# Kernel tuning notes

Hardware: AMD Instinct MI355X
Metric: run time of the kernel (lower is better)

The kernel has to match this reference:

```python
import jax, jax.numpy as jnp
import numpy as np

B, T, D_MODEL, N_HEAD = 1, 2048, 768, 12
D_HEAD = D_MODEL // N_HEAD
D_HID = 4 * D_MODEL
EPS = 1e-6
ROPE_BASE = 10000.0


def _rms(x):
    # F.rms_norm with no learned weight (pre-norm, modded-nanogpt style)
    return x * jax.lax.rsqrt(jnp.mean(x * x, axis=-1, keepdims=True) + EPS)


def _rope(x, cos, sin):
    # x: (B, T, H, Dh); cos/sin: (1, T, 1, Dh//2)
    d = x.shape[-1] // 2
    x1, x2 = x[..., :d], x[..., d:]
    return jnp.concatenate([x1 * cos + x2 * sin, -x1 * sin + x2 * cos], axis=-1)


def setup_inputs() -> dict:
    key = jax.random.key(0)
    ks = jax.random.split(key, 11)
    w = lambda k, shape: (jax.random.normal(k, shape, jnp.float32) * 0.02)
    return {
        "x": jax.random.normal(ks[0], (B, T, D_MODEL), jnp.float32),
        "Wq": w(ks[1], (D_MODEL, D_MODEL)),
        "Wk": w(ks[2], (D_MODEL, D_MODEL)),
        "Wq2": w(ks[3], (D_MODEL, D_MODEL)),
        "Wk2": w(ks[4], (D_MODEL, D_MODEL)),
        "Wv": w(ks[5], (D_MODEL, D_MODEL)),
        "Wo": w(ks[6], (D_MODEL, D_MODEL)),
        "Wp1": w(ks[7], (D_HID, D_MODEL)),
        "Wp2": w(ks[8], (D_HID, D_MODEL)),
        "Wd": w(ks[9], (D_MODEL, D_HID)),
        "bd": jax.random.normal(ks[10], (D_MODEL,), jnp.float32) * 0.02,
    }


def reference(x, Wq, Wk, Wq2, Wk2, Wv, Wo, Wp1, Wp2, Wd, bd):
    Bb, Tt, C = x.shape
    H, Dh = N_HEAD, C // N_HEAD

    # --- CausalBilinearSelfAttention (pre-norm residual) ---
    h = _rms(x)
    proj = lambda W: (h @ W.T).reshape(Bb, Tt, H, Dh)
    q, k, q2, k2, v = proj(Wq), proj(Wk), proj(Wq2), proj(Wk2), proj(Wv)

    inv_freq = 1.0 / (ROPE_BASE ** (jnp.arange(0, Dh, 2, dtype=jnp.float32) / Dh))
    freqs = jnp.arange(Tt, dtype=jnp.float32)[:, None] * inv_freq[None, :]  # (T, Dh/2)
    cos = jnp.cos(freqs)[None, :, None, :]
    sin = jnp.sin(freqs)[None, :, None, :]
    q, k = _rope(q, cos, sin), _rope(k, cos, sin)
    q2, k2 = _rope(q2, cos, sin), _rope(k2, cos, sin)

    scores = jnp.einsum('bqhd,bkhd->bhqk', q, k)    # (B,H,T,T)
    scores2 = jnp.einsum('bqhd,bkhd->bhqk', q2, k2)  # (B,H,T,T)
    pattern = (scores / Dh) * (scores2 / Dh)
    causal = jnp.tril(jnp.ones((Tt, Tt), dtype=bool))
    pattern = jnp.where(causal, pattern, 0.0)
    z = jnp.einsum('bhqk,bkhd->bqhd', pattern, v).reshape(Bb, Tt, C)
    x = x + z @ Wo.T

    # --- BilinearLayer MLP (pre-norm residual) ---
    h2 = _rms(x)
    hidden = (h2 @ Wp1.T) * (h2 @ Wp2.T)
    x = x + (hidden @ Wd.T + bd)
    return x
```

## Files before the change

kernel.cpp:

```cpp
#include <hip/hip_runtime.h>
#include <hip/hip_bf16.h>

typedef __bf16 bf16;
typedef bf16 bf16x8 __attribute__((ext_vector_type(8)));
typedef float f32x4 __attribute__((ext_vector_type(4)));

#define MFMA16(a, b, c) __builtin_amdgcn_mfma_f32_16x16x32_bf16((a), (b), (c), 0, 0, 0)

static constexpr int TT    = 2048;
static constexpr int CC    = 768;
static constexpr int NHEAD = 12;
static constexpr int DHEAD = 64;

__device__ inline bf16x8 cvt8(const float4& a, const float4& b) {
    bf16x8 o;
    o[0] = (bf16)a.x; o[1] = (bf16)a.y; o[2] = (bf16)a.z; o[3] = (bf16)a.w;
    o[4] = (bf16)b.x; o[5] = (bf16)b.y; o[6] = (bf16)b.z; o[7] = (bf16)b.w;
    return o;
}

struct ConvArgs {
    const float* src[9];
    bf16*        dst[9];
    int          n[9];
};

__global__ __launch_bounds__(256) void convert_w(ConvArgs args) {
    int seg = blockIdx.y;
    int n   = args.n[seg];
    int i8  = (blockIdx.x * 256 + threadIdx.x) * 8;
    if (i8 >= n) return;
    const float4 a = *(const float4*)(args.src[seg] + i8);
    const float4 b = *(const float4*)(args.src[seg] + i8 + 4);
    *(bf16x8*)(args.dst[seg] + i8) = cvt8(a, b);
}

__global__ __launch_bounds__(256) void zero_f32(float* __restrict__ p) {
    int i = (blockIdx.x * 256 + threadIdx.x) * 4;
    *(f32x4*)(p + i) = f32x4{0.f, 0.f, 0.f, 0.f};
}

__global__ __launch_bounds__(256) void init_bias(const float* __restrict__ xmid,
                                                 const float* __restrict__ bd,
                                                 float* __restrict__ out) {
    int i4 = (blockIdx.x * 256 + threadIdx.x) * 4;
    int col = i4 % CC;
    float4 a = *(const float4*)(xmid + i4);
    float4 b = *(const float4*)(bd + col);
    *(float4*)(out + i4) = float4{a.x + b.x, a.y + b.y, a.z + b.z, a.w + b.w};
}

__global__ __launch_bounds__(256) void rope_table(float* __restrict__ cosT, float* __restrict__ sinT) {
    int i = blockIdx.x * 256 + threadIdx.x;
    int t = i >> 5, j = i & 31;
    float inv = 1.0f / powf(10000.0f, (float)(2 * j) / 64.0f);
    float f = (float)t * inv;
    cosT[i] = cosf(f);
    sinT[i] = sinf(f);
}

__global__ __launch_bounds__(256) void rmsnorm(const float* __restrict__ x, bf16* __restrict__ out) {
    int row = blockIdx.x;
    const float* xr = x + (long)row * CC;
    int tid = threadIdx.x;
    float v0 = xr[tid], v1 = xr[tid + 256], v2 = xr[tid + 512];
    float ss = v0 * v0 + v1 * v1 + v2 * v2;
    #pragma unroll
    for (int off = 32; off > 0; off >>= 1) ss += __shfl_down(ss, off);
    __shared__ float red[4];
    if ((tid & 63) == 0) red[tid >> 6] = ss;
    __syncthreads();
    float tot = red[0] + red[1] + red[2] + red[3];
    float sc = rsqrtf(tot * (1.0f / 768.0f) + 1e-6f);
    bf16* o = out + (long)row * CC;
    o[tid]       = (bf16)(v0 * sc);
    o[tid + 256] = (bf16)(v1 * sc);
    o[tid + 512] = (bf16)(v2 * sc);
}

template <int EPI, bool AF32, int BM, int BN, int SK>
__global__ __launch_bounds__(256) void gemm_bt(
    const void* __restrict__ Av, const bf16* __restrict__ B,
    bf16* __restrict__ outb, float* __restrict__ outf,
    const float* __restrict__ res, const float* __restrict__ bias,
    const float* __restrict__ cosT, const float* __restrict__ sinT,
    int M, int N, int K)
{
    constexpr int BK = 64, LDR = 72;
    constexpr int WC = BN / 64, WR = 4 / WC, FM = BM / (WR * 16);
    constexpr int RA = BM / 32, RB = BN / 32;
    __shared__ bf16 Al[BM * LDR];
    __shared__ bf16 Bl[BN * LDR];

    const int tid = threadIdx.x, lane = tid & 63, wave = tid >> 6;
    const int wr = wave / WC, wc = wave % WC;
    const int l15 = lane & 15, lhi = lane >> 4;
    const int bm = blockIdx.x * BM, bn = blockIdx.y * BN;

    const int srow = tid >> 3;
    const int scol = (tid & 7) * 8;

    const int kchunk = K / SK;
    const int koff   = (SK > 1) ? blockIdx.z * kchunk : 0;

    const bf16*  Ag  = (const bf16*)Av  + (long)(bm + srow) * K + koff + scol;
    const float* Agf = (const float*)Av + (long)(bm + srow) * K + koff + scol;
    const bf16*  Bg  = B + (long)(bn + srow) * K + koff + scol;

    f32x4 acc[FM][4] = {};
    const int nk = kchunk / BK;

    bf16x8 ga[RA], gb[RB];
    float4 fa[RA][2];
    auto LOAD = [&](int t) {
        #pragma unroll
        for (int i = 0; i < RA; ++i) {
            if constexpr (AF32) {
                const float* p = Agf + (long)i * 32 * K + t * BK;
                fa[i][0] = *(const float4*)(p);
                fa[i][1] = *(const float4*)(p + 4);
            } else {
                ga[i] = *(const bf16x8*)(Ag + (long)i * 32 * K + t * BK);
            }
        }
        #pragma unroll
        for (int i = 0; i < RB; ++i)
            gb[i] = *(const bf16x8*)(Bg + (long)i * 32 * K + t * BK);
    };
    LOAD(0);

    for (int t = 0; t < nk; ++t) {
        __syncthreads();
        #pragma unroll
        for (int i = 0; i < RA; ++i) {
            if constexpr (AF32)
                *(bf16x8*)(&Al[(srow + i * 32) * LDR + scol]) = cvt8(fa[i][0], fa[i][1]);
            else
                *(bf16x8*)(&Al[(srow + i * 32) * LDR + scol]) = ga[i];
        }
        #pragma unroll
        for (int i = 0; i < RB; ++i)
            *(bf16x8*)(&Bl[(srow + i * 32) * LDR + scol]) = gb[i];
        __syncthreads();
        if (t + 1 < nk) LOAD(t + 1);

        bf16x8 afr[FM][2], bfr[4][2];
        #pragma unroll
        for (int m = 0; m < FM; ++m)
            #pragma unroll
            for (int kk = 0; kk < 2; ++kk)
                afr[m][kk] = *(const bf16x8*)(&Al[(wr * FM * 16 + m * 16 + l15) * LDR + kk * 32 + lhi * 8]);
        #pragma unroll
        for (int n = 0; n < 4; ++n)
            #pragma unroll
            for (int kk = 0; kk < 2; ++kk)
                bfr[n][kk] = *(const bf16x8*)(&Bl[(wc * 64 + n * 16 + l15) * LDR + kk * 32 + lhi * 8]);
        #pragma unroll
        for (int kk = 0; kk < 2; ++kk)
            #pragma unroll
            for (int m = 0; m < FM; ++m)
                #pragma unroll
                for (int n = 0; n < 4; ++n)
                    acc[m][n] = MFMA16(afr[m][kk], bfr[n][kk], acc[m][n]);
    }

    if (EPI == 4) {
        const bool dorope = (bn < 3072);
        #pragma unroll
        for (int m = 0; m < FM; ++m) {
            int row0 = bm + wr * FM * 16 + m * 16 + lhi * 4;
            if (dorope) {
                #pragma unroll
                for (int n = 0; n < 2; ++n) {
                    int j   = n * 16 + l15;
                    int col = bn + wc * 64 + n * 16 + l15;
                    #pragma unroll
                    for (int r = 0; r < 4; ++r) {
                        int t = row0 + r;
                        float c = cosT[t * 32 + j], s = sinT[t * 32 + j];
                        float a = acc[m][n][r], b = acc[m][n + 2][r];
                        outb[(long)t * N + col]      = (bf16)(a * c + b * s);
                        outb[(long)t * N + col + 32] = (bf16)(-a * s + b * c);
                    }
                }
            } else {
                #pragma unroll
                for (int n = 0; n < 4; ++n) {
                    int col = bn + wc * 64 + n * 16 + l15;
                    #pragma unroll
                    for (int r = 0; r < 4; ++r)
                        outb[(long)(row0 + r) * N + col] = (bf16)acc[m][n][r];
                }
            }
        }
        return;
    }

    #pragma unroll
    for (int m = 0; m < FM; ++m) {
        #pragma unroll
        for (int n = 0; n < 4; ++n) {
            int row0 = bm + wr * FM * 16 + m * 16 + lhi * 4;
            int col  = bn + wc * 64 + n * 16 + l15;
            #pragma unroll
            for (int r = 0; r < 4; ++r) {
                long idx = (long)(row0 + r) * N + col;
                float v = acc[m][n][r];
                if (EPI == 0) {
                    outb[idx] = (bf16)v;
                } else if (EPI == 1) {
                    outf[idx] = res[idx] + v;
                } else if (EPI == 2) {
                    outf[idx] = res[idx] + bias[col] + v;
                } else {
                    atomicAdd(&outf[idx], v);
                }
            }
        }
    }
}

__global__ __launch_bounds__(256) void gemm_mlp_up(
    const bf16* __restrict__ A, const bf16* __restrict__ B1, const bf16* __restrict__ B2,
    bf16* __restrict__ out, int M, int N, int K)
{
    constexpr int BK = 64, LDR = 72;
    __shared__ bf16 Al[64 * LDR];
    __shared__ bf16 B1l[128 * LDR];
    __shared__ bf16 B2l[128 * LDR];

    const int tid = threadIdx.x, lane = tid & 63, wave = tid >> 6;
    const int wr = wave >> 1, wc = wave & 1;
    const int l15 = lane & 15, lhi = lane >> 4;
    const int bm = blockIdx.x * 64, bn = blockIdx.y * 128;

    const int srow = tid >> 3;
    const int scol = (tid & 7) * 8;

    const bf16* Ag  = A  + (long)(bm + srow) * K + scol;
    const bf16* B1g = B1 + (long)(bn + srow) * K + scol;
    const bf16* B2g = B2 + (long)(bn + srow) * K + scol;

    f32x4 acc1[2][4] = {};
    f32x4 acc2[2][4] = {};
    const int nk = K / BK;

    bf16x8 ga[2], g1[4], g2[4];
    auto LOAD = [&](int t) {
        #pragma unroll
        for (int i = 0; i < 2; ++i)
            ga[i] = *(const bf16x8*)(Ag + (long)i * 32 * K + t * BK);
        #pragma unroll
        for (int i = 0; i < 4; ++i) {
            g1[i] = *(const bf16x8*)(B1g + (long)i * 32 * K + t * BK);
            g2[i] = *(const bf16x8*)(B2g + (long)i * 32 * K + t * BK);
        }
    };
    LOAD(0);

    for (int t = 0; t < nk; ++t) {
        __syncthreads();
        #pragma unroll
        for (int i = 0; i < 2; ++i)
            *(bf16x8*)(&Al[(srow + i * 32) * LDR + scol]) = ga[i];
        #pragma unroll
        for (int i = 0; i < 4; ++i) {
            *(bf16x8*)(&B1l[(srow + i * 32) * LDR + scol]) = g1[i];
            *(bf16x8*)(&B2l[(srow + i * 32) * LDR + scol]) = g2[i];
        }
        __syncthreads();
        if (t + 1 < nk) LOAD(t + 1);

        bf16x8 a[2][2], b1[4][2], b2[4][2];
        #pragma unroll
        for (int m = 0; m < 2; ++m)
            #pragma unroll
            for (int kk = 0; kk < 2; ++kk)
                a[m][kk] = *(const bf16x8*)(&Al[(wr * 32 + m * 16 + l15) * LDR + kk * 32 + lhi * 8]);
        #pragma unroll
        for (int n = 0; n < 4; ++n)
            #pragma unroll
            for (int kk = 0; kk < 2; ++kk) {
                b1[n][kk] = *(const bf16x8*)(&B1l[(wc * 64 + n * 16 + l15) * LDR + kk * 32 + lhi * 8]);
                b2[n][kk] = *(const bf16x8*)(&B2l[(wc * 64 + n * 16 + l15) * LDR + kk * 32 + lhi * 8]);
            }
        #pragma unroll
        for (int kk = 0; kk < 2; ++kk)
            #pragma unroll
            for (int m = 0; m < 2; ++m)
                #pragma unroll
                for (int n = 0; n < 4; ++n) {
                    acc1[m][n] = MFMA16(a[m][kk], b1[n][kk], acc1[m][n]);
                    acc2[m][n] = MFMA16(a[m][kk], b2[n][kk], acc2[m][n]);
                }
    }

    #pragma unroll
    for (int m = 0; m < 2; ++m) {
        #pragma unroll
        for (int n = 0; n < 4; ++n) {
            int row0 = bm + wr * 32 + m * 16 + lhi * 4;
            int col  = bn + wc * 64 + n * 16 + l15;
            #pragma unroll
            for (int r = 0; r < 4; ++r)
                out[(long)(row0 + r) * N + col] = (bf16)(acc1[m][n][r] * acc2[m][n][r]);
        }
    }
}

__global__ __launch_bounds__(512) void attn(const bf16* __restrict__ qkv, float* __restrict__ z) {
    constexpr int LDK = 72, LDV = 66, LDP = 72;
    __shared__ bf16 Kl[64 * LDK];
    __shared__ bf16 K2l[64 * LDK];
    __shared__ bf16 Vt[64 * LDV];
    __shared__ bf16 Pl[8][16 * LDP];

    const int qtb = 15 - blockIdx.x, h = blockIdx.y, s = blockIdx.z;
    const int nkt = 2 * qtb + 2;
    const int cb = nkt >> 2, rem = nkt & 3;
    const int len = cb + (s < rem ? 1 : 0);
    if (len == 0) return;
    const int k0 = s * cb + min(s, rem);

    const int tid = threadIdx.x, lane = tid & 63, wave = tid >> 6;
    const int l15 = lane & 15, lhi = lane >> 4;
    const int q0w = qtb * 128 + wave * 16;
    const int wkt0 = q0w >> 6;

    const bf16* qbase = qkv + (long)(q0w + l15) * 3840 + h * DHEAD + lhi * 8;
    const bf16x8 qa0  = *(const bf16x8*)(qbase);
    const bf16x8 qa1  = *(const bf16x8*)(qbase + 32);
    const bf16x8 q2a0 = *(const bf16x8*)(qbase + 1536);
    const bf16x8 q2a1 = *(const bf16x8*)(qbase + 1536 + 32);

    f32x4 zacc[4] = {};

    const int srow = tid >> 3;
    const int scol = (tid & 7) * 8;

    bf16x8 kvr, k2r, vvr;
    auto LOAD = [&](int kt) {
        const bf16* src = qkv + (long)(kt * 64 + srow) * 3840 + h * DHEAD + scol;
        kvr = *(const bf16x8*)(src + 768);
        k2r = *(const bf16x8*)(src + 2304);
        vvr = *(const bf16x8*)(src + 3072);
    };
    LOAD(k0);

    for (int kt = k0; kt < k0 + len; ++kt) {
        __syncthreads();
        *(bf16x8*)(&Kl[srow * LDK + scol])  = kvr;
        *(bf16x8*)(&K2l[srow * LDK + scol]) = k2r;
        #pragma unroll
        for (int e = 0; e < 8; ++e) Vt[(scol + e) * LDV + srow] = vvr[e];
        __syncthreads();
        if (kt + 1 < k0 + len) LOAD(kt + 1);

        if (kt > wkt0) continue;
        const bool diag = (kt == wkt0);

        f32x4 s1[4] = {}, s2[4] = {};
        #pragma unroll
        for (int nf = 0; nf < 4; ++nf) {
            bf16x8 kb0 = *(const bf16x8*)(&Kl[(nf * 16 + l15) * LDK + lhi * 8]);
            s1[nf] = MFMA16(qa0, kb0, s1[nf]);
            bf16x8 kb1 = *(const bf16x8*)(&Kl[(nf * 16 + l15) * LDK + 32 + lhi * 8]);
            s1[nf] = MFMA16(qa1, kb1, s1[nf]);
            bf16x8 k2b0 = *(const bf16x8*)(&K2l[(nf * 16 + l15) * LDK + lhi * 8]);
            s2[nf] = MFMA16(q2a0, k2b0, s2[nf]);
            bf16x8 k2b1 = *(const bf16x8*)(&K2l[(nf * 16 + l15) * LDK + 32 + lhi * 8]);
            s2[nf] = MFMA16(q2a1, k2b1, s2[nf]);
        }

        #pragma unroll
        for (int nf = 0; nf < 4; ++nf) {
            #pragma unroll
            for (int r = 0; r < 4; ++r) {
                float p = s1[nf][r] * s2[nf][r] * (1.0f / 4096.0f);
                if (diag) {
                    int qg = q0w + lhi * 4 + r;
                    int kg = kt * 64 + nf * 16 + l15;
                    p = (kg <= qg) ? p : 0.0f;
                }
                Pl[wave][(lhi * 4 + r) * LDP + nf * 16 + l15] = (bf16)p;
            }
        }

        #pragma unroll
        for (int kk = 0; kk < 2; ++kk) {
            bf16x8 pa = *(const bf16x8*)(&Pl[wave][l15 * LDP + kk * 32 + lhi * 8]);
            #pragma unroll
            for (int f = 0; f < 4; ++f) {
                bf16x8 vb = *(const bf16x8*)(&Vt[(f * 16 + l15) * LDV + kk * 32 + lhi * 8]);
                zacc[f] = MFMA16(pa, vb, zacc[f]);
            }
        }
    }

    if (k0 <= wkt0) {
        #pragma unroll
        for (int f = 0; f < 4; ++f) {
            #pragma unroll
            for (int r = 0; r < 4; ++r) {
                atomicAdd(&z[(long)(q0w + lhi * 4 + r) * CC + h * DHEAD + f * 16 + l15], zacc[f][r]);
            }
        }
    }
}

extern "C" void kernel_launch(void* const* d_in, const int* in_sizes, int n_in,
                              void* d_out, int out_size, void* d_ws, size_t ws_size,
                              hipStream_t stream) {
    const float* x   = (const float*)d_in[0];
    const float* Wq  = (const float*)d_in[1];
    const float* Wk  = (const float*)d_in[2];
    const float* Wq2 = (const float*)d_in[3];
    const float* Wk2 = (const float*)d_in[4];
    const float* Wv  = (const float*)d_in[5];
    const float* Wo  = (const float*)d_in[6];
    const float* Wp1 = (const float*)d_in[7];
    const float* Wp2 = (const float*)d_in[8];
    const float* Wd  = (const float*)d_in[9];
    const float* bd  = (const float*)d_in[10];

    char* ws = (char*)d_ws;
    size_t off = 0;
    auto alloc = [&](size_t bytes) {
        void* p = ws + off;
        off += (bytes + 255) & ~(size_t)255;
        return p;
    };
    bf16*  Wall  = (bf16*)alloc(10616832l * 2);
    float* xmid  = (float*)alloc(2048l * 768 * 4);
    bf16*  h2    = (bf16*)alloc(2048l * 768 * 2);
    bf16*  hid   = (bf16*)alloc(2048l * 3072 * 2);
    bf16*  h1    = (bf16*)alloc(2048l * 768 * 2);
    float* cosT  = (float*)alloc(2048l * 32 * 4);
    float* sinT  = (float*)alloc(2048l * 32 * 4);
    bf16*  qkv   = (bf16*)alloc(2048l * 3840 * 2);
    float* zbuf  = (float*)hid;

    const long SW = 589824;
    bf16* Wqkvb = Wall;
    bf16* Wob   = Wall + 5 * SW;
    bf16* Wp1b  = Wall + 6 * SW;
    bf16* Wp2b  = Wp1b + 2359296;
    bf16* Wdb   = Wp2b + 2359296;

    ConvArgs ca;
    const float* wsrc[9] = {Wq, Wk, Wq2, Wk2, Wv, Wo, Wp1, Wp2, Wd};
    bf16* wdst[9] = {Wqkvb, Wqkvb + SW, Wqkvb + 2 * SW, Wqkvb + 3 * SW, Wqkvb + 4 * SW,
                     Wob, Wp1b, Wp2b, Wdb};
    int wn[9] = {589824, 589824, 589824, 589824, 589824, 589824, 2359296, 2359296, 2359296};
    for (int i = 0; i < 9; ++i) { ca.src[i] = wsrc[i]; ca.dst[i] = wdst[i]; ca.n[i] = wn[i]; }

    convert_w<<<dim3(1152, 9), 256, 0, stream>>>(ca);
    rope_table<<<dim3(256), 256, 0, stream>>>(cosT, sinT);
    rmsnorm<<<dim3(2048), 256, 0, stream>>>(x, h1);
    gemm_bt<4, false, 128, 128, 1><<<dim3(16, 30), 256, 0, stream>>>(
        h1, Wqkvb, qkv, nullptr, nullptr, nullptr, cosT, sinT, 2048, 3840, 768);
    zero_f32<<<dim3(1536), 256, 0, stream>>>(zbuf);
    attn<<<dim3(16, 12, 4), 512, 0, stream>>>(qkv, zbuf);
    hipMemcpyAsync(xmid, x, 2048l * 768 * 4, hipMemcpyDeviceToDevice, stream);
    gemm_bt<3, true, 64, 64, 2><<<dim3(32, 12, 2), 256, 0, stream>>>(
        zbuf, Wob, nullptr, xmid, nullptr, nullptr, nullptr, nullptr, 2048, 768, 768);
    rmsnorm<<<dim3(2048), 256, 0, stream>>>(xmid, h2);
    gemm_mlp_up<<<dim3(32, 24), 256, 0, stream>>>(h2, Wp1b, Wp2b, hid, 2048, 3072, 768);
    init_bias<<<dim3(1536), 256, 0, stream>>>(xmid, bd, (float*)d_out);
    gemm_bt<3, false, 64, 64, 2><<<dim3(32, 12, 2), 256, 0, stream>>>(
        hid, Wdb, nullptr, (float*)d_out, nullptr, nullptr, nullptr, nullptr, 2048, 768, 3072);
}
```

Measured before the change: 250.2 us.

## Fold zbuf zeroing into weight convert, double-buffer attn K/V, fuse residual into Wo GEMM

```diff
diff --git a/kernel.cpp b/kernel.cpp
--- a/kernel.cpp
+++ b/kernel.cpp
@@ -20,9 +20,9 @@
 }
 
 struct ConvArgs {
-    const float* src[9];
-    bf16*        dst[9];
-    int          n[9];
+    const float* src[10];
+    bf16*        dst[10];
+    int          n[10];
 };
 
 __global__ __launch_bounds__(256) void convert_w(ConvArgs args) {
@@ -30,14 +30,13 @@
     int n   = args.n[seg];
     int i8  = (blockIdx.x * 256 + threadIdx.x) * 8;
     if (i8 >= n) return;
+    if (args.src[seg] == nullptr) {
+        *(bf16x8*)(args.dst[seg] + i8) = bf16x8{};
+        return;
+    }
     const float4 a = *(const float4*)(args.src[seg] + i8);
     const float4 b = *(const float4*)(args.src[seg] + i8 + 4);
     *(bf16x8*)(args.dst[seg] + i8) = cvt8(a, b);
-}
-
-__global__ __launch_bounds__(256) void zero_f32(float* __restrict__ p) {
-    int i = (blockIdx.x * 256 + threadIdx.x) * 4;
-    *(f32x4*)(p + i) = f32x4{0.f, 0.f, 0.f, 0.f};
 }
 
 __global__ __launch_bounds__(256) void init_bias(const float* __restrict__ xmid,
@@ -310,9 +309,9 @@
 
 __global__ __launch_bounds__(512) void attn(const bf16* __restrict__ qkv, float* __restrict__ z) {
     constexpr int LDK = 72, LDV = 66, LDP = 72;
-    __shared__ bf16 Kl[64 * LDK];
-    __shared__ bf16 K2l[64 * LDK];
-    __shared__ bf16 Vt[64 * LDV];
+    __shared__ bf16 Kl[2][64 * LDK];
+    __shared__ bf16 K2l[2][64 * LDK];
+    __shared__ bf16 Vt[2][64 * LDV];
     __shared__ bf16 Pl[8][16 * LDP];
 
     const int qtb = 15 - blockIdx.x, h = blockIdx.y, s = blockIdx.z;
@@ -347,12 +346,12 @@
     };
     LOAD(k0);
 
-    for (int kt = k0; kt < k0 + len; ++kt) {
-        __syncthreads();
-        *(bf16x8*)(&Kl[srow * LDK + scol])  = kvr;
-        *(bf16x8*)(&K2l[srow * LDK + scol]) = k2r;
-        #pragma unroll
-        for (int e = 0; e < 8; ++e) Vt[(scol + e) * LDV + srow] = vvr[e];
+    int cur = 0;
+    for (int kt = k0; kt < k0 + len; ++kt, cur ^= 1) {
+        *(bf16x8*)(&Kl[cur][srow * LDK + scol])  = kvr;
+        *(bf16x8*)(&K2l[cur][srow * LDK + scol]) = k2r;
+        #pragma unroll
+        for (int e = 0; e < 8; ++e) Vt[cur][(scol + e) * LDV + srow] = vvr[e];
         __syncthreads();
         if (kt + 1 < k0 + len) LOAD(kt + 1);
 
@@ -362,13 +361,13 @@
         f32x4 s1[4] = {}, s2[4] = {};
         #pragma unroll
         for (int nf = 0; nf < 4; ++nf) {
-            bf16x8 kb0 = *(const bf16x8*)(&Kl[(nf * 16 + l15) * LDK + lhi * 8]);
+            bf16x8 kb0 = *(const bf16x8*)(&Kl[cur][(nf * 16 + l15) * LDK + lhi * 8]);
             s1[nf] = MFMA16(qa0, kb0, s1[nf]);
-            bf16x8 kb1 = *(const bf16x8*)(&Kl[(nf * 16 + l15) * LDK + 32 + lhi * 8]);
+            bf16x8 kb1 = *(const bf16x8*)(&Kl[cur][(nf * 16 + l15) * LDK + 32 + lhi * 8]);
             s1[nf] = MFMA16(qa1, kb1, s1[nf]);
-            bf16x8 k2b0 = *(const bf16x8*)(&K2l[(nf * 16 + l15) * LDK + lhi * 8]);
+            bf16x8 k2b0 = *(const bf16x8*)(&K2l[cur][(nf * 16 + l15) * LDK + lhi * 8]);
             s2[nf] = MFMA16(q2a0, k2b0, s2[nf]);
-            bf16x8 k2b1 = *(const bf16x8*)(&K2l[(nf * 16 + l15) * LDK + 32 + lhi * 8]);
+            bf16x8 k2b1 = *(const bf16x8*)(&K2l[cur][(nf * 16 + l15) * LDK + 32 + lhi * 8]);
             s2[nf] = MFMA16(q2a1, k2b1, s2[nf]);
         }
 
@@ -391,7 +390,7 @@
             bf16x8 pa = *(const bf16x8*)(&Pl[wave][l15 * LDP + kk * 32 + lhi * 8]);
             #pragma unroll
             for (int f = 0; f < 4; ++f) {
-                bf16x8 vb = *(const bf16x8*)(&Vt[(f * 16 + l15) * LDV + kk * 32 + lhi * 8]);
+                bf16x8 vb = *(const bf16x8*)(&Vt[cur][(f * 16 + l15) * LDV + kk * 32 + lhi * 8]);
                 zacc[f] = MFMA16(pa, vb, zacc[f]);
             }
         }
@@ -448,22 +447,21 @@
     bf16* Wdb   = Wp2b + 2359296;
 
     ConvArgs ca;
-    const float* wsrc[9] = {Wq, Wk, Wq2, Wk2, Wv, Wo, Wp1, Wp2, Wd};
-    bf16* wdst[9] = {Wqkvb, Wqkvb + SW, Wqkvb + 2 * SW, Wqkvb + 3 * SW, Wqkvb + 4 * SW,
-                     Wob, Wp1b, Wp2b, Wdb};
-    int wn[9] = {589824, 589824, 589824, 589824, 589824, 589824, 2359296, 2359296, 2359296};
-    for (int i = 0; i < 9; ++i) { ca.src[i] = wsrc[i]; ca.dst[i] = wdst[i]; ca.n[i] = wn[i]; }
-
-    convert_w<<<dim3(1152, 9), 256, 0, stream>>>(ca);
+    const float* wsrc[10] = {Wq, Wk, Wq2, Wk2, Wv, Wo, Wp1, Wp2, Wd, nullptr};
+    bf16* wdst[10] = {Wqkvb, Wqkvb + SW, Wqkvb + 2 * SW, Wqkvb + 3 * SW, Wqkvb + 4 * SW,
+                      Wob, Wp1b, Wp2b, Wdb, (bf16*)zbuf};
+    int wn[10] = {589824, 589824, 589824, 589824, 589824, 589824,
+                  2359296, 2359296, 2359296, 3145728};
+    for (int i = 0; i < 10; ++i) { ca.src[i] = wsrc[i]; ca.dst[i] = wdst[i]; ca.n[i] = wn[i]; }
+
+    convert_w<<<dim3(1536, 10), 256, 0, stream>>>(ca);
     rope_table<<<dim3(256), 256, 0, stream>>>(cosT, sinT);
     rmsnorm<<<dim3(2048), 256, 0, stream>>>(x, h1);
     gemm_bt<4, false, 128, 128, 1><<<dim3(16, 30), 256, 0, stream>>>(
         h1, Wqkvb, qkv, nullptr, nullptr, nullptr, cosT, sinT, 2048, 3840, 768);
-    zero_f32<<<dim3(1536), 256, 0, stream>>>(zbuf);
     attn<<<dim3(16, 12, 4), 512, 0, stream>>>(qkv, zbuf);
-    hipMemcpyAsync(xmid, x, 2048l * 768 * 4, hipMemcpyDeviceToDevice, stream);
-    gemm_bt<3, true, 64, 64, 2><<<dim3(32, 12, 2), 256, 0, stream>>>(
-        zbuf, Wob, nullptr, xmid, nullptr, nullptr, nullptr, nullptr, 2048, 768, 768);
+    gemm_bt<1, true, 64, 64, 1><<<dim3(32, 12), 256, 0, stream>>>(
+        zbuf, Wob, nullptr, xmid, x, nullptr, nullptr, nullptr, 2048, 768, 768);
     rmsnorm<<<dim3(2048), 256, 0, stream>>>(xmid, h2);
     gemm_mlp_up<<<dim3(32, 24), 256, 0, stream>>>(h2, Wp1b, Wp2b, hid, 2048, 3072, 768);
     init_bias<<<dim3(1536), 256, 0, stream>>>(xmid, bd, (float*)d_out);
```

Measured after the change: 239.8 us. -4.1%, faster.
